# Performance work log

Measured on AMD Instinct MI355X. Metric: run time of the kernel, lower is better.

## Reference

```python
import jax, jax.numpy as jnp
import numpy as np
from jax import lax


def setup_inputs() -> dict:
    key = jax.random.key(0)
    ks = jax.random.split(key, 20)
    B, D, T = 1024, 256, 128
    H, O = 256, 64
    f32 = jnp.float32
    rn = lambda k, shape, sc: jax.random.normal(k, shape, f32) * sc
    ru = lambda k, shape: jax.random.uniform(k, shape, f32)
    return {
        "x": jax.random.normal(ks[0], (B, D, T), f32),
        "W_in": rn(ks[1], (H, D), 1.0 / np.sqrt(D)),
        "b_in": rn(ks[2], (H,), 0.02),
        "beta1": ru(ks[3], (H,)),
        "thr1": ru(ks[4], (H,)),
        "W_h": rn(ks[5], (H, H), 1.0 / np.sqrt(H)),
        "b_h": rn(ks[6], (H,), 0.02),
        "beta2": ru(ks[7], (H,)),
        "thr2": ru(ks[8], (H,)),
        "W_h1": rn(ks[9], (H, H), 1.0 / np.sqrt(H)),
        "b_h1": rn(ks[10], (H,), 0.02),
        "W_f": rn(ks[11], (O, H), 1.0 / np.sqrt(H)),
        "b_f": rn(ks[12], (O,), 0.02),
        "beta_f": ru(ks[13], (O,)),
        "W_a": rn(ks[14], (O, H), 1.0 / np.sqrt(H)),
        "b_a": rn(ks[15], (O,), 0.02),
        "beta_a": ru(ks[16], (O,)),
    }


def _spike(u):
    # heaviside(u > 0); surrogate grad only matters in backward
    return (u > 0).astype(u.dtype)


def reference(x, W_in, b_in, beta1, thr1, W_h, b_h, beta2, thr2,
              W_h1, b_h1, W_f, b_f, beta_f, W_a, b_a, beta_a):
    B = x.shape[0]
    H0, H1, H2 = W_in.shape[0], W_h.shape[0], W_h1.shape[0]
    O = W_f.shape[0]
    dt = x.dtype
    # snntorch clamps learnable beta to [0, 1] in the state update
    b1c = jnp.clip(beta1, 0.0, 1.0)
    b2c = jnp.clip(beta2, 0.0, 1.0)
    bfc = jnp.clip(beta_f, 0.0, 1.0)
    bac = jnp.clip(beta_a, 0.0, 1.0)
    xT = jnp.transpose(x, (2, 0, 1))  # [T, B, D]

    def lif(mem, cur, bc, thr):
        # snntorch Leaky, reset_mechanism='subtract': reset from PREVIOUS mem (detached)
        reset = lax.stop_gradient(_spike(mem - thr))
        mem = bc * mem + cur - reset * thr
        spk = _spike(mem - thr)
        return spk, mem

    def step(carry, xt):
        m1, m2, m3, mf, ma = carry
        cur1 = xt @ W_in.T + b_in
        s1, m1 = lif(m1, cur1, b1c, thr1)
        cur2 = s1 @ W_h.T + b_h
        s2, m2 = lif(m2, cur2, b2c, thr2)
        # source bug preserved: third layer reuses lif_hidden (beta2, thr2)
        cur3 = s2 @ W_h1.T + b_h1
        s3, m3 = lif(m3, cur3, b2c, thr2)
        # output LI neurons: reset_mechanism='none'
        mf = bfc * mf + (s3 @ W_f.T + b_f)
        ma = bac * ma + (s3 @ W_a.T + b_a)
        return (m1, m2, m3, mf, ma), None

    z = lambda n: jnp.zeros((B, n), dt)
    init = (z(H0), z(H1), z(H2), z(O), z(O))
    (m1, m2, m3, mf, ma), _ = lax.scan(step, init, xT)
    return jax.nn.sigmoid(mf), jax.nn.sigmoid(ma)
```

## Files before the change

kernel.cpp:

```cpp
#include <hip/hip_runtime.h>
#include <math.h>
#include <stdint.h>


namespace {

constexpr int Bsz = 1024;
constexpr int Dd  = 256;
constexpr int Tt  = 128;
constexpr int Hh  = 256;
constexpr int Oo  = 64;

__global__ void pack_t(const float* __restrict__ W, float* __restrict__ Wt,
                       int R, int C) {
    int idx = blockIdx.x * 256 + threadIdx.x;
    if (idx >= (C + 1) * R) return;
    int c = idx / R, r = idx - c * R;
    Wt[idx] = (c < C) ? W[(size_t)r * C + c] : 0.f;
}

__global__ void pack_o(const float* __restrict__ Wf, const float* __restrict__ Wa,
                       float* __restrict__ WtO) {
    int idx = blockIdx.x * 256 + threadIdx.x;
    if (idx >= 257 * 128) return;
    int k = idx >> 7, o = idx & 127;
    float v = 0.f;
    if (k < 256) v = (o < 64) ? Wf[(size_t)o * 256 + k] : Wa[(size_t)(o - 64) * 256 + k];
    WtO[idx] = v;
}

__device__ __forceinline__ float clamp01(float v) { return fminf(fmaxf(v, 0.f), 1.f); }

__device__ __forceinline__ bool lif_step(float& m, float cur, float B, float Th) {
    const float r = (__fsub_rn(m, Th) > 0.f) ? Th : 0.f;
    m = __fsub_rn(__fadd_rn(__fmul_rn(B, m), cur), r);
    return __fsub_rn(m, Th) > 0.f;
}

__device__ __forceinline__ void make_masks(int nib, int lane, uint64_t* M) {
    #pragma unroll
    for (int q = 0; q < 4; ++q) {
        const int v   = __shfl(nib, 16 * q + (lane >> 2), 64);
        const int bit = (v >> (lane & 3)) & 1;
        M[q] = __ballot(bit != 0);
    }
}

__device__ __forceinline__ int compact(int nib, int lane, const uint64_t* M,
                                       uint16_t* lst) {
    const int p0 = (int)__popcll(M[0]);
    const int p1 = (int)__popcll(M[1]);
    const int p2 = (int)__popcll(M[2]);
    const int p3 = (int)__popcll(M[3]);
    const int q  = lane >> 4;
    const int base = ((q >= 1) ? p0 : 0) + ((q >= 2) ? p1 : 0) + ((q >= 3) ? p2 : 0);
    const uint64_t mq = (q & 2) ? ((q & 1) ? M[3] : M[2])
                                : ((q & 1) ? M[1] : M[0]);
    const int posb = (lane & 15) << 2;
    const int r0 = base + (int)__popcll(mq & ((1ull << posb) - 1ull));
    const int s1 = nib & 1;
    const int s2 = s1 + ((nib >> 1) & 1);
    const int s3 = s2 + ((nib >> 2) & 1);
    const int nb = lane << 2;
    if (nib & 1) lst[r0]      = (uint16_t)nb;
    if (nib & 2) lst[r0 + s1] = (uint16_t)(nb + 1);
    if (nib & 4) lst[r0 + s2] = (uint16_t)(nb + 2);
    if (nib & 8) lst[r0 + s3] = (uint16_t)(nb + 3);
    const int n    = p0 + p1 + p2 + p3;
    const int npad = (n + 7) & ~7;
    if (lane < npad - n) lst[n + lane] = (uint16_t)Hh;
    return npad;
}


__device__ __forceinline__ void issue8h(const char* __restrict__ tab,
                                        uint4 I, int offB, float4* w) {
    const int k[8] = {(int)(I.x & 0xffff), (int)(I.x >> 16),
                      (int)(I.y & 0xffff), (int)(I.y >> 16),
                      (int)(I.z & 0xffff), (int)(I.z >> 16),
                      (int)(I.w & 0xffff), (int)(I.w >> 16)};
    #pragma unroll
    for (int i = 0; i < 8; ++i)
        w[i] = *(const float4*)(tab + (k[i] << 10) + offB);
}

__device__ __forceinline__ void cons8h(float4& c, const float4* w) {
    #pragma unroll
    for (int i = 0; i < 8; ++i) {
        c.x = __fadd_rn(c.x, w[i].x);
        c.y = __fadd_rn(c.y, w[i].y);
        c.z = __fadd_rn(c.z, w[i].z);
        c.w = __fadd_rn(c.w, w[i].w);
    }
}

__device__ __forceinline__ float4 sum_h(const uint16_t* lst, int nbat,
                                        const float* __restrict__ tab, int offB) {
    float4 c = {0.f, 0.f, 0.f, 0.f};
    if (nbat == 0) return c;
    const char* tb = (const char*)tab;
    float4 A[8], B[8];
    issue8h(tb, *(const uint4*)(lst), offB, A);
    int i = 1;
    for (; i + 1 < nbat; i += 2) {
        issue8h(tb, *(const uint4*)(lst + 8 * i), offB, B);
        cons8h(c, A);
        issue8h(tb, *(const uint4*)(lst + 8 * (i + 1)), offB, A);
        cons8h(c, B);
    }
    if (i < nbat) {
        issue8h(tb, *(const uint4*)(lst + 8 * i), offB, B);
        cons8h(c, A);
        cons8h(c, B);
    } else {
        cons8h(c, A);
    }
    return c;
}


__device__ __forceinline__ void issue8o(const char* __restrict__ tab,
                                        uint4 I, int offB, float2* w) {
    const int k[8] = {(int)(I.x & 0xffff), (int)(I.x >> 16),
                      (int)(I.y & 0xffff), (int)(I.y >> 16),
                      (int)(I.z & 0xffff), (int)(I.z >> 16),
                      (int)(I.w & 0xffff), (int)(I.w >> 16)};
    #pragma unroll
    for (int i = 0; i < 8; ++i)
        w[i] = *(const float2*)(tab + (k[i] << 9) + offB);
}

__device__ __forceinline__ void cons8o(float2& c, const float2* w) {
    #pragma unroll
    for (int i = 0; i < 8; ++i) {
        c.x = __fadd_rn(c.x, w[i].x);
        c.y = __fadd_rn(c.y, w[i].y);
    }
}

__device__ __forceinline__ float2 sum_o(const uint16_t* lst, int nbat,
                                        const float* __restrict__ tab, int offB) {
    float2 c = {0.f, 0.f};
    if (nbat == 0) return c;
    const char* tb = (const char*)tab;
    float2 A[8], B[8];
    issue8o(tb, *(const uint4*)(lst), offB, A);
    int i = 1;
    for (; i + 1 < nbat; i += 2) {
        issue8o(tb, *(const uint4*)(lst + 8 * i), offB, B);
        cons8o(c, A);
        issue8o(tb, *(const uint4*)(lst + 8 * (i + 1)), offB, A);
        cons8o(c, B);
    }
    if (i < nbat) {
        issue8o(tb, *(const uint4*)(lst + 8 * i), offB, B);
        cons8o(c, A);
        cons8o(c, B);
    } else {
        cons8o(c, A);
    }
    return c;
}

__global__ __launch_bounds__(256, 1) void snn_rec(
    const float* __restrict__ cur1,
    const float* __restrict__ Wt_h, const float* __restrict__ Wt_h1,
    const float* __restrict__ WtO,
    const float* __restrict__ beta1, const float* __restrict__ thr1,
    const float* __restrict__ b_h,  const float* __restrict__ beta2, const float* __restrict__ thr2,
    const float* __restrict__ b_h1,
    const float* __restrict__ b_f,  const float* __restrict__ beta_f,
    const float* __restrict__ b_a,  const float* __restrict__ beta_a,
    float* __restrict__ m1s, float* __restrict__ m2s, float* __restrict__ m3s,
    float* __restrict__ mos, float* __restrict__ out,
    int TC, int first)
{
    __shared__ __attribute__((aligned(16))) uint16_t lists[4][272];

    const int tid  = threadIdx.x;
    const int lane = tid & 63;
    const int b    = blockIdx.x * 4 + (tid >> 6);
    uint16_t* lst  = lists[tid >> 6];
    const int off4 = lane * 4;
    const int off2 = lane * 2;
    const int offBh = lane * 16;
    const int offBo = lane * 8;

    const float4 B1v  = *(const float4*)(beta1 + off4);
    const float4 Th1v = *(const float4*)(thr1  + off4);
    const float4 bhv  = *(const float4*)(b_h   + off4);
    const float4 B2v  = *(const float4*)(beta2 + off4);
    const float4 Th2v = *(const float4*)(thr2  + off4);
    const float4 bh1v = *(const float4*)(b_h1  + off4);
    const float4 B1c  = {clamp01(B1v.x), clamp01(B1v.y), clamp01(B1v.z), clamp01(B1v.w)};
    const float4 B2c  = {clamp01(B2v.x), clamp01(B2v.y), clamp01(B2v.z), clamp01(B2v.w)};

    const int oo = off2 & 63;
    const float* bop = (lane < 32) ? b_f    : b_a;
    const float* Bop = (lane < 32) ? beta_f : beta_a;
    const float bo0 = bop[oo], bo1 = bop[oo + 1];
    const float Bo0 = clamp01(Bop[oo]), Bo1 = clamp01(Bop[oo + 1]);

    float4 m1, m2, m3;
    float mo0, mo1;
    if (first) {
        m1 = m2 = m3 = make_float4(0.f, 0.f, 0.f, 0.f);
        mo0 = mo1 = 0.f;
    } else {
        m1 = *(const float4*)(m1s + (size_t)b * Hh + off4);
        m2 = *(const float4*)(m2s + (size_t)b * Hh + off4);
        m3 = *(const float4*)(m3s + (size_t)b * Hh + off4);
        const float2 mo = *(const float2*)(mos + (size_t)b * 128 + off2);
        mo0 = mo.x; mo1 = mo.y;
    }

    const float* __restrict__ curb = cur1 + (size_t)b * TC * Hh + off4;
    float4 cur = *(const float4*)(curb);
    uint64_t M[4];

    for (int t = 0; t < TC; ++t) {
        int nib = 0;
        nib |= (int)lif_step(m1.x, cur.x, B1c.x, Th1v.x);
        nib |= (int)lif_step(m1.y, cur.y, B1c.y, Th1v.y) << 1;
        nib |= (int)lif_step(m1.z, cur.z, B1c.z, Th1v.z) << 2;
        nib |= (int)lif_step(m1.w, cur.w, B1c.w, Th1v.w) << 3;
        make_masks(nib, lane, M);
        int npad = compact(nib, lane, M, lst);
        if (t + 1 < TC) cur = *(const float4*)(curb + (size_t)(t + 1) * Hh);

        float4 s = sum_h(lst, npad >> 3, Wt_h, offBh);
        nib  = (int)lif_step(m2.x, __fadd_rn(s.x, bhv.x), B2c.x, Th2v.x);
        nib |= (int)lif_step(m2.y, __fadd_rn(s.y, bhv.y), B2c.y, Th2v.y) << 1;
        nib |= (int)lif_step(m2.z, __fadd_rn(s.z, bhv.z), B2c.z, Th2v.z) << 2;
        nib |= (int)lif_step(m2.w, __fadd_rn(s.w, bhv.w), B2c.w, Th2v.w) << 3;
        make_masks(nib, lane, M);
        npad = compact(nib, lane, M, lst);

        s = sum_h(lst, npad >> 3, Wt_h1, offBh);
        nib  = (int)lif_step(m3.x, __fadd_rn(s.x, bh1v.x), B2c.x, Th2v.x);
        nib |= (int)lif_step(m3.y, __fadd_rn(s.y, bh1v.y), B2c.y, Th2v.y) << 1;
        nib |= (int)lif_step(m3.z, __fadd_rn(s.z, bh1v.z), B2c.z, Th2v.z) << 2;
        nib |= (int)lif_step(m3.w, __fadd_rn(s.w, bh1v.w), B2c.w, Th2v.w) << 3;
        make_masks(nib, lane, M);
        npad = compact(nib, lane, M, lst);

        const float2 os = sum_o(lst, npad >> 3, WtO, offBo);
        mo0 = __fadd_rn(__fmul_rn(Bo0, mo0), __fadd_rn(os.x, bo0));
        mo1 = __fadd_rn(__fmul_rn(Bo1, mo1), __fadd_rn(os.y, bo1));
    }

    *(float4*)(m1s + (size_t)b * Hh + off4) = m1;
    *(float4*)(m2s + (size_t)b * Hh + off4) = m2;
    *(float4*)(m3s + (size_t)b * Hh + off4) = m3;
    *(float2*)(mos + (size_t)b * 128 + off2) = make_float2(mo0, mo1);

    float* dst = out + ((lane < 32) ? 0 : (size_t)Bsz * Oo) + (size_t)b * Oo + oo;
    const float o0 = (float)(1.0 / (1.0 + exp(-(double)mo0)));
    const float o1 = (float)(1.0 / (1.0 + exp(-(double)mo1)));
    *(float2*)dst = make_float2(o0, o1);
}

template<int TT>
__global__ __launch_bounds__(256) void gemm_l1_lds(
    const float* __restrict__ x, const float* __restrict__ Wt_in,
    const float* __restrict__ b_in, float* __restrict__ cur1,
    int tg_base, int TCloc)
{
    __shared__ float xs[Dd][TT];
    const int h   = threadIdx.x;
    const int b   = blockIdx.x;
    const int ty  = blockIdx.y;
    const int tg0 = tg_base + ty * TT;
    const float* xb = x + (size_t)b * Dd * Tt + tg0;
    constexpr int T4 = TT / 4;
    for (int v = threadIdx.x; v < Dd * T4; v += 256) {
        const int d = v / T4, j4 = v - d * T4;
        *(float4*)&xs[d][j4 * 4] = *(const float4*)(xb + (size_t)d * Tt + j4 * 4);
    }
    __syncthreads();
    float c[TT];
    #pragma unroll
    for (int j = 0; j < TT; ++j) c[j] = 0.f;
    for (int d = 0; d < Dd; ++d) {
        const float w = Wt_in[d * Hh + h];
        #pragma unroll
        for (int j = 0; j < TT; ++j) c[j] = fmaf(w, xs[d][j], c[j]);
    }
    const float bb = b_in[h];
    float* cb = cur1 + ((size_t)b * TCloc + ty * TT) * Hh;
    #pragma unroll
    for (int j = 0; j < TT; ++j) cb[j * Hh + h] = __fadd_rn(c[j], bb);
}

template<int TT>
__global__ __launch_bounds__(256) void gemm_l1_simple(
    const float* __restrict__ x, const float* __restrict__ Wt_in,
    const float* __restrict__ b_in, float* __restrict__ cur1, int tg0)
{
    const int h = threadIdx.x;
    const int b = blockIdx.x;
    float c[TT];
    #pragma unroll
    for (int j = 0; j < TT; ++j) c[j] = 0.f;
    const float* xb = x + (size_t)b * Dd * Tt + tg0;
    for (int d = 0; d < Dd; ++d) {
        const float w = Wt_in[d * Hh + h];
        const float* xp = xb + (size_t)d * Tt;
        #pragma unroll
        for (int j = 0; j < TT; ++j) c[j] = fmaf(w, xp[j], c[j]);
    }
    const float bb = b_in[h];
    float* cb = cur1 + (size_t)b * TT * Hh;
    #pragma unroll
    for (int j = 0; j < TT; ++j) cb[j * Hh + h] = __fadd_rn(c[j], bb);
}

}

extern "C" void kernel_launch(void* const* d_in, const int* in_sizes, int n_in,
                              void* d_out, int out_size, void* d_ws, size_t ws_size,
                              hipStream_t stream) {
    const float* x      = (const float*)d_in[0];
    const float* W_in   = (const float*)d_in[1];
    const float* b_in   = (const float*)d_in[2];
    const float* beta1  = (const float*)d_in[3];
    const float* thr1   = (const float*)d_in[4];
    const float* W_h    = (const float*)d_in[5];
    const float* b_h    = (const float*)d_in[6];
    const float* beta2  = (const float*)d_in[7];
    const float* thr2   = (const float*)d_in[8];
    const float* W_h1   = (const float*)d_in[9];
    const float* b_h1   = (const float*)d_in[10];
    const float* W_f    = (const float*)d_in[11];
    const float* b_f    = (const float*)d_in[12];
    const float* beta_f = (const float*)d_in[13];
    const float* W_a    = (const float*)d_in[14];
    const float* b_a    = (const float*)d_in[15];
    const float* beta_a = (const float*)d_in[16];
    float* out = (float*)d_out;

    float* ws = (float*)d_ws;
    size_t off = 0;
    auto alloc = [&](size_t n) { float* p = ws + off; off += n; return p; };
    float* Wt_in = alloc(257 * 256);
    float* Wt_h  = alloc(257 * 256);
    float* Wt_h1 = alloc(257 * 256);
    float* WtO   = alloc(257 * 128);
    float* m1s   = alloc((size_t)Bsz * Hh);
    float* m2s   = alloc((size_t)Bsz * Hh);
    float* m3s   = alloc((size_t)Bsz * Hh);
    float* mos   = alloc((size_t)Bsz * 128);
    const size_t fixed = off;

    int TC = 1;
    const int cands[8] = {128, 64, 32, 16, 8, 4, 2, 1};
    for (int i = 0; i < 8; ++i) {
        if ((fixed + (size_t)cands[i] * Bsz * Hh) * sizeof(float) <= ws_size) { TC = cands[i]; break; }
    }
    float* cur1 = alloc((size_t)TC * Bsz * Hh);

    pack_t<<<257, 256, 0, stream>>>(W_in, Wt_in, 256, 256);
    pack_t<<<257, 256, 0, stream>>>(W_h,  Wt_h,  256, 256);
    pack_t<<<257, 256, 0, stream>>>(W_h1, Wt_h1, 256, 256);
    pack_o<<<129, 256, 0, stream>>>(W_f, W_a, WtO);

    const int nch = Tt / TC;
    for (int c = 0; c < nch; ++c) {
        const int tg = c * TC;
        if (TC >= 32)
            gemm_l1_lds<32><<<dim3(Bsz, TC / 32), 256, 0, stream>>>(x, Wt_in, b_in, cur1, tg, TC);
        else if (TC == 16)
            gemm_l1_lds<16><<<dim3(Bsz, 1), 256, 0, stream>>>(x, Wt_in, b_in, cur1, tg, TC);
        else if (TC == 8)
            gemm_l1_lds<8><<<dim3(Bsz, 1), 256, 0, stream>>>(x, Wt_in, b_in, cur1, tg, TC);
        else if (TC == 4)
            gemm_l1_simple<4><<<Bsz, 256, 0, stream>>>(x, Wt_in, b_in, cur1, tg);
        else if (TC == 2)
            gemm_l1_simple<2><<<Bsz, 256, 0, stream>>>(x, Wt_in, b_in, cur1, tg);
        else
            gemm_l1_simple<1><<<Bsz, 256, 0, stream>>>(x, Wt_in, b_in, cur1, tg);

        snn_rec<<<Bsz / 4, 256, 0, stream>>>(
            cur1, Wt_h, Wt_h1, WtO,
            beta1, thr1, b_h, beta2, thr2, b_h1,
            b_f, beta_f, b_a, beta_a,
            m1s, m2s, m3s, mos, out, TC, (c == 0) ? 1 : 0);
    }
}
```

Baseline: 1.352 ms.

## Deepen gather pipeline, store pre-shifted byte offsets, add register-tiled layer-1 GEMM

The sparse spike lists now hold 32-bit byte offsets precomputed at compaction time, which removes the shift and unpack work inside the gather loop. Batches are padded to 32 entries so the weight-row sum can keep four batches of loads in flight instead of two. The next timestep's input current load is issued earlier so it overlaps with the mask and gather work. A new layer-1 GEMM kernel gives each thread 4 hidden units by 8 timesteps held in registers. The costs are more padding work for sparse layers, higher register pressure and twice the LDS footprint for the lists.

```diff
diff --git a/kernel.cpp b/kernel.cpp
--- a/kernel.cpp
+++ b/kernel.cpp
@@ -46,8 +46,9 @@
     }
 }
 
+template<int SH>
 __device__ __forceinline__ int compact(int nib, int lane, const uint64_t* M,
-                                       uint16_t* lst) {
+                                       uint32_t* lst) {
     const int p0 = (int)__popcll(M[0]);
     const int p1 = (int)__popcll(M[1]);
     const int p2 = (int)__popcll(M[2]);
@@ -62,26 +63,30 @@
     const int s2 = s1 + ((nib >> 1) & 1);
     const int s3 = s2 + ((nib >> 2) & 1);
     const int nb = lane << 2;
-    if (nib & 1) lst[r0]      = (uint16_t)nb;
-    if (nib & 2) lst[r0 + s1] = (uint16_t)(nb + 1);
-    if (nib & 4) lst[r0 + s2] = (uint16_t)(nb + 2);
-    if (nib & 8) lst[r0 + s3] = (uint16_t)(nb + 3);
+    if (nib & 1) lst[r0]      = (uint32_t)(nb << SH);
+    if (nib & 2) lst[r0 + s1] = (uint32_t)((nb + 1) << SH);
+    if (nib & 4) lst[r0 + s2] = (uint32_t)((nb + 2) << SH);
+    if (nib & 8) lst[r0 + s3] = (uint32_t)((nb + 3) << SH);
     const int n    = p0 + p1 + p2 + p3;
-    const int npad = (n + 7) & ~7;
-    if (lane < npad - n) lst[n + lane] = (uint16_t)Hh;
+    const int npad = (n + 31) & ~31;
+    if (lane < npad - n) lst[n + lane] = (uint32_t)(Hh << SH);
     return npad;
 }
 
 
 __device__ __forceinline__ void issue8h(const char* __restrict__ tab,
-                                        uint4 I, int offB, float4* w) {
-    const int k[8] = {(int)(I.x & 0xffff), (int)(I.x >> 16),
-                      (int)(I.y & 0xffff), (int)(I.y >> 16),
-                      (int)(I.z & 0xffff), (int)(I.z >> 16),
-                      (int)(I.w & 0xffff), (int)(I.w >> 16)};
-    #pragma unroll
-    for (int i = 0; i < 8; ++i)
-        w[i] = *(const float4*)(tab + (k[i] << 10) + offB);
+                                        const uint32_t* __restrict__ e, int offB,
+                                        float4* w) {
+    const uint4 I0 = *(const uint4*)(e);
+    const uint4 I1 = *(const uint4*)(e + 4);
+    w[0] = *(const float4*)(tab + I0.x + offB);
+    w[1] = *(const float4*)(tab + I0.y + offB);
+    w[2] = *(const float4*)(tab + I0.z + offB);
+    w[3] = *(const float4*)(tab + I0.w + offB);
+    w[4] = *(const float4*)(tab + I1.x + offB);
+    w[5] = *(const float4*)(tab + I1.y + offB);
+    w[6] = *(const float4*)(tab + I1.z + offB);
+    w[7] = *(const float4*)(tab + I1.w + offB);
 }
 
 __device__ __forceinline__ void cons8h(float4& c, const float4* w) {
@@ -94,40 +99,40 @@
     }
 }
 
-__device__ __forceinline__ float4 sum_h(const uint16_t* lst, int nbat,
+__device__ __forceinline__ float4 sum_h(const uint32_t* lst, int nbat,
                                         const float* __restrict__ tab, int offB) {
     float4 c = {0.f, 0.f, 0.f, 0.f};
     if (nbat == 0) return c;
     const char* tb = (const char*)tab;
-    float4 A[8], B[8];
-    issue8h(tb, *(const uint4*)(lst), offB, A);
-    int i = 1;
-    for (; i + 1 < nbat; i += 2) {
-        issue8h(tb, *(const uint4*)(lst + 8 * i), offB, B);
-        cons8h(c, A);
-        issue8h(tb, *(const uint4*)(lst + 8 * (i + 1)), offB, A);
-        cons8h(c, B);
-    }
-    if (i < nbat) {
-        issue8h(tb, *(const uint4*)(lst + 8 * i), offB, B);
-        cons8h(c, A);
-        cons8h(c, B);
-    } else {
-        cons8h(c, A);
-    }
+    float4 WA[8], WB[8], WC[8], WD[8];
+    issue8h(tb, lst +  0, offB, WA);
+    issue8h(tb, lst +  8, offB, WB);
+    issue8h(tb, lst + 16, offB, WC);
+    issue8h(tb, lst + 24, offB, WD);
+    for (int i = 4; i < nbat; i += 4) {
+        cons8h(c, WA); issue8h(tb, lst + 8 * i,       offB, WA);
+        cons8h(c, WB); issue8h(tb, lst + 8 * (i + 1), offB, WB);
+        cons8h(c, WC); issue8h(tb, lst + 8 * (i + 2), offB, WC);
+        cons8h(c, WD); issue8h(tb, lst + 8 * (i + 3), offB, WD);
+    }
+    cons8h(c, WA); cons8h(c, WB); cons8h(c, WC); cons8h(c, WD);
     return c;
 }
 
 
 __device__ __forceinline__ void issue8o(const char* __restrict__ tab,
-                                        uint4 I, int offB, float2* w) {
-    const int k[8] = {(int)(I.x & 0xffff), (int)(I.x >> 16),
-                      (int)(I.y & 0xffff), (int)(I.y >> 16),
-                      (int)(I.z & 0xffff), (int)(I.z >> 16),
-                      (int)(I.w & 0xffff), (int)(I.w >> 16)};
-    #pragma unroll
-    for (int i = 0; i < 8; ++i)
-        w[i] = *(const float2*)(tab + (k[i] << 9) + offB);
+                                        const uint32_t* __restrict__ e, int offB,
+                                        float2* w) {
+    const uint4 I0 = *(const uint4*)(e);
+    const uint4 I1 = *(const uint4*)(e + 4);
+    w[0] = *(const float2*)(tab + I0.x + offB);
+    w[1] = *(const float2*)(tab + I0.y + offB);
+    w[2] = *(const float2*)(tab + I0.z + offB);
+    w[3] = *(const float2*)(tab + I0.w + offB);
+    w[4] = *(const float2*)(tab + I1.x + offB);
+    w[5] = *(const float2*)(tab + I1.y + offB);
+    w[6] = *(const float2*)(tab + I1.z + offB);
+    w[7] = *(const float2*)(tab + I1.w + offB);
 }
 
 __device__ __forceinline__ void cons8o(float2& c, const float2* w) {
@@ -138,27 +143,23 @@
     }
 }
 
-__device__ __forceinline__ float2 sum_o(const uint16_t* lst, int nbat,
+__device__ __forceinline__ float2 sum_o(const uint32_t* lst, int nbat,
                                         const float* __restrict__ tab, int offB) {
     float2 c = {0.f, 0.f};
     if (nbat == 0) return c;
     const char* tb = (const char*)tab;
-    float2 A[8], B[8];
-    issue8o(tb, *(const uint4*)(lst), offB, A);
-    int i = 1;
-    for (; i + 1 < nbat; i += 2) {
-        issue8o(tb, *(const uint4*)(lst + 8 * i), offB, B);
-        cons8o(c, A);
-        issue8o(tb, *(const uint4*)(lst + 8 * (i + 1)), offB, A);
-        cons8o(c, B);
-    }
-    if (i < nbat) {
-        issue8o(tb, *(const uint4*)(lst + 8 * i), offB, B);
-        cons8o(c, A);
-        cons8o(c, B);
-    } else {
-        cons8o(c, A);
-    }
+    float2 WA[8], WB[8], WC[8], WD[8];
+    issue8o(tb, lst +  0, offB, WA);
+    issue8o(tb, lst +  8, offB, WB);
+    issue8o(tb, lst + 16, offB, WC);
+    issue8o(tb, lst + 24, offB, WD);
+    for (int i = 4; i < nbat; i += 4) {
+        cons8o(c, WA); issue8o(tb, lst + 8 * i,       offB, WA);
+        cons8o(c, WB); issue8o(tb, lst + 8 * (i + 1), offB, WB);
+        cons8o(c, WC); issue8o(tb, lst + 8 * (i + 2), offB, WC);
+        cons8o(c, WD); issue8o(tb, lst + 8 * (i + 3), offB, WD);
+    }
+    cons8o(c, WA); cons8o(c, WB); cons8o(c, WC); cons8o(c, WD);
     return c;
 }
 
@@ -175,12 +176,12 @@
     float* __restrict__ mos, float* __restrict__ out,
     int TC, int first)
 {
-    __shared__ __attribute__((aligned(16))) uint16_t lists[4][272];
+    __shared__ __attribute__((aligned(16))) uint32_t lists[4][256];
 
     const int tid  = threadIdx.x;
     const int lane = tid & 63;
     const int b    = blockIdx.x * 4 + (tid >> 6);
-    uint16_t* lst  = lists[tid >> 6];
+    uint32_t* lst  = lists[tid >> 6];
     const int off4 = lane * 4;
     const int off2 = lane * 2;
     const int offBh = lane * 16;
@@ -224,9 +225,10 @@
         nib |= (int)lif_step(m1.y, cur.y, B1c.y, Th1v.y) << 1;
         nib |= (int)lif_step(m1.z, cur.z, B1c.z, Th1v.z) << 2;
         nib |= (int)lif_step(m1.w, cur.w, B1c.w, Th1v.w) << 3;
+        float4 curN;
+        if (t + 1 < TC) curN = *(const float4*)(curb + (size_t)(t + 1) * Hh);
         make_masks(nib, lane, M);
-        int npad = compact(nib, lane, M, lst);
-        if (t + 1 < TC) cur = *(const float4*)(curb + (size_t)(t + 1) * Hh);
+        int npad = compact<10>(nib, lane, M, lst);
 
         float4 s = sum_h(lst, npad >> 3, Wt_h, offBh);
         nib  = (int)lif_step(m2.x, __fadd_rn(s.x, bhv.x), B2c.x, Th2v.x);
@@ -234,7 +236,7 @@
         nib |= (int)lif_step(m2.z, __fadd_rn(s.z, bhv.z), B2c.z, Th2v.z) << 2;
         nib |= (int)lif_step(m2.w, __fadd_rn(s.w, bhv.w), B2c.w, Th2v.w) << 3;
         make_masks(nib, lane, M);
-        npad = compact(nib, lane, M, lst);
+        npad = compact<10>(nib, lane, M, lst);
 
         s = sum_h(lst, npad >> 3, Wt_h1, offBh);
         nib  = (int)lif_step(m3.x, __fadd_rn(s.x, bh1v.x), B2c.x, Th2v.x);
@@ -242,11 +244,12 @@
         nib |= (int)lif_step(m3.z, __fadd_rn(s.z, bh1v.z), B2c.z, Th2v.z) << 2;
         nib |= (int)lif_step(m3.w, __fadd_rn(s.w, bh1v.w), B2c.w, Th2v.w) << 3;
         make_masks(nib, lane, M);
-        npad = compact(nib, lane, M, lst);
+        npad = compact<9>(nib, lane, M, lst);
 
         const float2 os = sum_o(lst, npad >> 3, WtO, offBo);
         mo0 = __fadd_rn(__fmul_rn(Bo0, mo0), __fadd_rn(os.x, bo0));
         mo1 = __fadd_rn(__fmul_rn(Bo1, mo1), __fadd_rn(os.y, bo1));
+        cur = curN;
     }
 
     *(float4*)(m1s + (size_t)b * Hh + off4) = m1;
@@ -258,6 +261,56 @@
     const float o0 = (float)(1.0 / (1.0 + exp(-(double)mo0)));
     const float o1 = (float)(1.0 / (1.0 + exp(-(double)mo1)));
     *(float2*)dst = make_float2(o0, o1);
+}
+
+template<int TT>
+__global__ __launch_bounds__(256) void gemm_l1_r8(
+    const float* __restrict__ x, const float* __restrict__ Wt_in,
+    const float* __restrict__ b_in, float* __restrict__ cur1,
+    int tg_base, int TCloc)
+{
+    __shared__ float xs[Dd][TT];
+    const int tid = threadIdx.x;
+    const int b   = blockIdx.x;
+    const int ty  = blockIdx.y;
+    const int tg0 = tg_base + ty * TT;
+    const float* xb = x + (size_t)b * Dd * Tt + tg0;
+    constexpr int T4 = TT / 4;
+    for (int v = tid; v < Dd * T4; v += 256) {
+        const int d = v / T4, j4 = v - d * T4;
+        *(float4*)&xs[d][j4 * 4] = *(const float4*)(xb + (size_t)d * Tt + j4 * 4);
+    }
+    __syncthreads();
+    constexpr int TS = TT / 4;
+    const int hq = tid & 63;
+    const int tq = tid >> 6;
+    float c0[TS], c1[TS], c2[TS], c3[TS];
+    #pragma unroll
+    for (int j = 0; j < TS; ++j) { c0[j] = 0.f; c1[j] = 0.f; c2[j] = 0.f; c3[j] = 0.f; }
+    const float* wp = Wt_in + hq * 4;
+    #pragma unroll 4
+    for (int d = 0; d < Dd; ++d) {
+        const float4 w = *(const float4*)(wp + (size_t)d * Hh);
+        #pragma unroll
+        for (int j = 0; j < TS; ++j) {
+            const float xv = xs[d][tq * TS + j];
+            c0[j] = fmaf(w.x, xv, c0[j]);
+            c1[j] = fmaf(w.y, xv, c1[j]);
+            c2[j] = fmaf(w.z, xv, c2[j]);
+            c3[j] = fmaf(w.w, xv, c3[j]);
+        }
+    }
+    const float4 bb = *(const float4*)(b_in + hq * 4);
+    float* cb = cur1 + ((size_t)b * TCloc + ty * TT + tq * TS) * Hh + hq * 4;
+    #pragma unroll
+    for (int j = 0; j < TS; ++j) {
+        float4 o;
+        o.x = __fadd_rn(c0[j], bb.x);
+        o.y = __fadd_rn(c1[j], bb.y);
+        o.z = __fadd_rn(c2[j], bb.z);
+        o.w = __fadd_rn(c3[j], bb.w);
+        *(float4*)(cb + (size_t)j * Hh) = o;
+    }
 }
 
 template<int TT>
@@ -368,7 +421,7 @@
     for (int c = 0; c < nch; ++c) {
         const int tg = c * TC;
         if (TC >= 32)
-            gemm_l1_lds<32><<<dim3(Bsz, TC / 32), 256, 0, stream>>>(x, Wt_in, b_in, cur1, tg, TC);
+            gemm_l1_r8<32><<<dim3(Bsz, TC / 32), 256, 0, stream>>>(x, Wt_in, b_in, cur1, tg, TC);
         else if (TC == 16)
             gemm_l1_lds<16><<<dim3(Bsz, 1), 256, 0, stream>>>(x, Wt_in, b_in, cur1, tg, TC);
         else if (TC == 8)
```

After: 1.365 ms. No clear change (+0.9%).

## Stage output weights in LDS, triple-buffer hidden gathers, register-blocked input GEMM

Applied to the files above, without the earlier changes.

The recurrent kernel now copies the packed output-layer weight table (about 128KB) into shared memory once per block and gathers from LDS instead of global memory. The hidden-layer sparse gather is deepened from double to triple buffering, with scheduling barriers to keep loads in flight. A new layer-1 GEMM kernel register-blocks four hidden units by eight timesteps per thread to cut LDS reads per FMA. The large LDS allocation limits occupancy to one block per CU and adds a preload cost, and the deeper buffering raises register pressure.

```diff
diff --git a/kernel.cpp b/kernel.cpp
--- a/kernel.cpp
+++ b/kernel.cpp
@@ -99,65 +99,57 @@
     float4 c = {0.f, 0.f, 0.f, 0.f};
     if (nbat == 0) return c;
     const char* tb = (const char*)tab;
-    float4 A[8], B[8];
+    float4 A[8], B[8], C[8];
     issue8h(tb, *(const uint4*)(lst), offB, A);
-    int i = 1;
-    for (; i + 1 < nbat; i += 2) {
-        issue8h(tb, *(const uint4*)(lst + 8 * i), offB, B);
-        cons8h(c, A);
-        issue8h(tb, *(const uint4*)(lst + 8 * (i + 1)), offB, A);
-        cons8h(c, B);
-    }
-    if (i < nbat) {
-        issue8h(tb, *(const uint4*)(lst + 8 * i), offB, B);
-        cons8h(c, A);
-        cons8h(c, B);
+    if (nbat == 1) { cons8h(c, A); return c; }
+    issue8h(tb, *(const uint4*)(lst + 8), offB, B);
+    if (nbat == 2) { cons8h(c, A); cons8h(c, B); return c; }
+    issue8h(tb, *(const uint4*)(lst + 16), offB, C);
+    __builtin_amdgcn_sched_barrier(0);
+    int i = 3;
+    for (; i + 2 < nbat; i += 3) {
+        cons8h(c, A); issue8h(tb, *(const uint4*)(lst + 8 * i), offB, A);
+        __builtin_amdgcn_sched_barrier(0);
+        cons8h(c, B); issue8h(tb, *(const uint4*)(lst + 8 * (i + 1)), offB, B);
+        __builtin_amdgcn_sched_barrier(0);
+        cons8h(c, C); issue8h(tb, *(const uint4*)(lst + 8 * (i + 2)), offB, C);
+        __builtin_amdgcn_sched_barrier(0);
+    }
+    const int r = nbat - i;
+    if (r == 0) {
+        cons8h(c, A); cons8h(c, B); cons8h(c, C);
+    } else if (r == 1) {
+        cons8h(c, A); issue8h(tb, *(const uint4*)(lst + 8 * i), offB, A);
+        cons8h(c, B); cons8h(c, C); cons8h(c, A);
     } else {
-        cons8h(c, A);
+        cons8h(c, A); issue8h(tb, *(const uint4*)(lst + 8 * i), offB, A);
+        cons8h(c, B); issue8h(tb, *(const uint4*)(lst + 8 * (i + 1)), offB, B);
+        cons8h(c, C); cons8h(c, A); cons8h(c, B);
     }
     return c;
 }
 
 
-__device__ __forceinline__ void issue8o(const char* __restrict__ tab,
-                                        uint4 I, int offB, float2* w) {
-    const int k[8] = {(int)(I.x & 0xffff), (int)(I.x >> 16),
-                      (int)(I.y & 0xffff), (int)(I.y >> 16),
-                      (int)(I.z & 0xffff), (int)(I.z >> 16),
-                      (int)(I.w & 0xffff), (int)(I.w >> 16)};
-    #pragma unroll
-    for (int i = 0; i < 8; ++i)
-        w[i] = *(const float2*)(tab + (k[i] << 9) + offB);
-}
-
-__device__ __forceinline__ void cons8o(float2& c, const float2* w) {
-    #pragma unroll
-    for (int i = 0; i < 8; ++i) {
-        c.x = __fadd_rn(c.x, w[i].x);
-        c.y = __fadd_rn(c.y, w[i].y);
-    }
-}
-
-__device__ __forceinline__ float2 sum_o(const uint16_t* lst, int nbat,
-                                        const float* __restrict__ tab, int offB) {
+__device__ __forceinline__ float2 sum_o_lds(const uint16_t* lst, int nbat,
+                                            const float* tab, int offB) {
     float2 c = {0.f, 0.f};
-    if (nbat == 0) return c;
     const char* tb = (const char*)tab;
-    float2 A[8], B[8];
-    issue8o(tb, *(const uint4*)(lst), offB, A);
-    int i = 1;
-    for (; i + 1 < nbat; i += 2) {
-        issue8o(tb, *(const uint4*)(lst + 8 * i), offB, B);
-        cons8o(c, A);
-        issue8o(tb, *(const uint4*)(lst + 8 * (i + 1)), offB, A);
-        cons8o(c, B);
-    }
-    if (i < nbat) {
-        issue8o(tb, *(const uint4*)(lst + 8 * i), offB, B);
-        cons8o(c, A);
-        cons8o(c, B);
-    } else {
-        cons8o(c, A);
+    for (int i = 0; i < nbat; ++i) {
+        const uint4 I = *(const uint4*)(lst + 8 * i);
+        float2 w[8];
+        w[0] = *(const float2*)(tb + ((I.x & 0xffffu) << 9) + offB);
+        w[1] = *(const float2*)(tb + ((I.x >> 16)    << 9) + offB);
+        w[2] = *(const float2*)(tb + ((I.y & 0xffffu) << 9) + offB);
+        w[3] = *(const float2*)(tb + ((I.y >> 16)    << 9) + offB);
+        w[4] = *(const float2*)(tb + ((I.z & 0xffffu) << 9) + offB);
+        w[5] = *(const float2*)(tb + ((I.z >> 16)    << 9) + offB);
+        w[6] = *(const float2*)(tb + ((I.w & 0xffffu) << 9) + offB);
+        w[7] = *(const float2*)(tb + ((I.w >> 16)    << 9) + offB);
+        #pragma unroll
+        for (int j = 0; j < 8; ++j) {
+            c.x = __fadd_rn(c.x, w[j].x);
+            c.y = __fadd_rn(c.y, w[j].y);
+        }
     }
     return c;
 }
@@ -175,6 +167,7 @@
     float* __restrict__ mos, float* __restrict__ out,
     int TC, int first)
 {
+    __shared__ __attribute__((aligned(16))) float ldsO[257 * 128];
     __shared__ __attribute__((aligned(16))) uint16_t lists[4][272];
 
     const int tid  = threadIdx.x;
@@ -185,6 +178,13 @@
     const int off2 = lane * 2;
     const int offBh = lane * 16;
     const int offBo = lane * 8;
+
+    {
+        const float4* s4 = (const float4*)WtO;
+        float4* d4 = (float4*)ldsO;
+        for (int v = tid; v < (257 * 128) / 4; v += 256) d4[v] = s4[v];
+    }
+    __syncthreads();
 
     const float4 B1v  = *(const float4*)(beta1 + off4);
     const float4 Th1v = *(const float4*)(thr1  + off4);
@@ -244,7 +244,7 @@
         make_masks(nib, lane, M);
         npad = compact(nib, lane, M, lst);
 
-        const float2 os = sum_o(lst, npad >> 3, WtO, offBo);
+        const float2 os = sum_o_lds(lst, npad >> 3, ldsO, offBo);
         mo0 = __fadd_rn(__fmul_rn(Bo0, mo0), __fadd_rn(os.x, bo0));
         mo1 = __fadd_rn(__fmul_rn(Bo1, mo1), __fadd_rn(os.y, bo1));
     }
@@ -258,6 +258,56 @@
     const float o0 = (float)(1.0 / (1.0 + exp(-(double)mo0)));
     const float o1 = (float)(1.0 / (1.0 + exp(-(double)mo1)));
     *(float2*)dst = make_float2(o0, o1);
+}
+
+template<int TT>
+__global__ __launch_bounds__(256) void gemm_l1_r8(
+    const float* __restrict__ x, const float* __restrict__ Wt_in,
+    const float* __restrict__ b_in, float* __restrict__ cur1,
+    int tg_base, int TCloc)
+{
+    __shared__ float xs[Dd][TT];
+    const int tid = threadIdx.x;
+    const int b   = blockIdx.x;
+    const int ty  = blockIdx.y;
+    const int tg0 = tg_base + ty * TT;
+    const float* xb = x + (size_t)b * Dd * Tt + tg0;
+    constexpr int T4 = TT / 4;
+    for (int v = tid; v < Dd * T4; v += 256) {
+        const int d = v / T4, j4 = v - d * T4;
+        *(float4*)&xs[d][j4 * 4] = *(const float4*)(xb + (size_t)d * Tt + j4 * 4);
+    }
+    __syncthreads();
+    constexpr int TS = TT / 4;
+    const int hq = tid & 63;
+    const int tq = tid >> 6;
+    float c0[TS], c1[TS], c2[TS], c3[TS];
+    #pragma unroll
+    for (int j = 0; j < TS; ++j) { c0[j] = 0.f; c1[j] = 0.f; c2[j] = 0.f; c3[j] = 0.f; }
+    const float* wp = Wt_in + hq * 4;
+    #pragma unroll 4
+    for (int d = 0; d < Dd; ++d) {
+        const float4 w = *(const float4*)(wp + (size_t)d * Hh);
+        #pragma unroll
+        for (int j = 0; j < TS; ++j) {
+            const float xv = xs[d][tq * TS + j];
+            c0[j] = fmaf(w.x, xv, c0[j]);
+            c1[j] = fmaf(w.y, xv, c1[j]);
+            c2[j] = fmaf(w.z, xv, c2[j]);
+            c3[j] = fmaf(w.w, xv, c3[j]);
+        }
+    }
+    const float4 bb = *(const float4*)(b_in + hq * 4);
+    float* cb = cur1 + ((size_t)b * TCloc + ty * TT + tq * TS) * Hh + hq * 4;
+    #pragma unroll
+    for (int j = 0; j < TS; ++j) {
+        float4 o;
+        o.x = __fadd_rn(c0[j], bb.x);
+        o.y = __fadd_rn(c1[j], bb.y);
+        o.z = __fadd_rn(c2[j], bb.z);
+        o.w = __fadd_rn(c3[j], bb.w);
+        *(float4*)(cb + (size_t)j * Hh) = o;
+    }
 }
 
 template<int TT>
@@ -368,7 +418,7 @@
     for (int c = 0; c < nch; ++c) {
         const int tg = c * TC;
         if (TC >= 32)
-            gemm_l1_lds<32><<<dim3(Bsz, TC / 32), 256, 0, stream>>>(x, Wt_in, b_in, cur1, tg, TC);
+            gemm_l1_r8<32><<<dim3(Bsz, TC / 32), 256, 0, stream>>>(x, Wt_in, b_in, cur1, tg, TC);
         else if (TC == 16)
             gemm_l1_lds<16><<<dim3(Bsz, 1), 256, 0, stream>>>(x, Wt_in, b_in, cur1, tg, TC);
         else if (TC == 8)
```

Measured after the change: 1.129 ms. 1.2x faster.
